# Kernel optimization log

Hardware: AMD Instinct MI355X
Metric: run time of the kernel (lower is better)

The kernel has to match this reference:

```python
import jax, jax.numpy as jnp
import numpy as np

DIM = 512
N_LAYERS = 2
N_HEADS = 8
HEAD_DIM = DIM // N_HEADS
VOCAB = 50257
MAX_SEQ = 2048
N_LEVELS = 3  # len(chunk_sizes)
HID = 4 * DIM
B, S = 2, 1024
STD = 0.02
EPS = 1e-5


def setup_inputs() -> dict:
    key = jax.random.key(0)
    ks = jax.random.split(key, 12)
    f32 = jnp.float32
    inp = {}
    inp["input_ids"] = jax.random.randint(ks[0], (B, S), 0, VOCAB)
    inp["tok_emb"] = jax.random.normal(ks[1], (VOCAB, DIM), f32) * STD  # tied with head
    inp["pos_emb"] = jax.random.normal(ks[2], (MAX_SEQ, DIM), f32) * STD
    # attention projections, stored [in, out] so y = x @ W (math-equivalent to torch x @ W.T)
    inp["Wq"] = jax.random.normal(ks[3], (N_LAYERS, DIM, DIM), f32) * STD
    inp["Wk"] = jax.random.normal(ks[4], (N_LAYERS, DIM, DIM), f32) * STD
    inp["Wv"] = jax.random.normal(ks[5], (N_LAYERS, DIM, DIM), f32) * STD
    inp["Wo"] = jax.random.normal(ks[6], (N_LAYERS, DIM, DIM), f32) * STD
    # layer norms
    inp["ln1_g"] = jnp.ones((N_LAYERS, DIM), f32)
    inp["ln1_b"] = jnp.zeros((N_LAYERS, DIM), f32)
    inp["ln2_g"] = jnp.ones((N_LAYERS, DIM), f32)
    inp["ln2_b"] = jnp.zeros((N_LAYERS, DIM), f32)
    inp["lnf_g"] = jnp.ones((DIM,), f32)
    inp["lnf_b"] = jnp.zeros((DIM,), f32)
    # continuum memory system: N_LEVELS chained MLPs per layer
    inp["W1"] = jax.random.normal(ks[7], (N_LAYERS, N_LEVELS, DIM, HID), f32) * STD
    inp["b1"] = jnp.zeros((N_LAYERS, N_LEVELS, HID), f32)
    inp["W2"] = jax.random.normal(ks[8], (N_LAYERS, N_LEVELS, HID, DIM), f32) * STD
    inp["b2"] = jnp.zeros((N_LAYERS, N_LEVELS, DIM), f32)
    return inp


def layer_norm(x, g, b):
    mu = jnp.mean(x, axis=-1, keepdims=True)
    var = jnp.var(x, axis=-1, keepdims=True)
    return (x - mu) / jnp.sqrt(var + EPS) * g + b


def linear_attention_with_memory(x, Wq, Wk, Wv, Wo):
    # x: [B, S, D]. Fast-weight recurrence: M_t = M_{t-1} + v_t k_t^T ; y_t = M_t q_t
    Bsz, Slen, D = x.shape
    H, hd = N_HEADS, HEAD_DIM

    def proj(W):  # -> [S, B, H, hd] (time-major for scan)
        return jnp.moveaxis((x @ W).reshape(Bsz, Slen, H, hd), 1, 0)

    q, k, v = proj(Wq), proj(Wk), proj(Wv)
    M0 = jnp.zeros((Bsz, H, hd, hd), x.dtype)

    def step(M, qkv):
        q_t, k_t, v_t = qkv
        M = M + jnp.einsum('bhd,bhk->bhdk', v_t, k_t)
        y_t = jnp.einsum('bhdk,bhk->bhd', M, q_t)
        return M, y_t

    _, ys = jax.lax.scan(step, M0, (q, k, v))  # ys: [S, B, H, hd]
    y = jnp.moveaxis(ys, 0, 1).reshape(Bsz, Slen, D)
    return y @ Wo


def cms(x, W1, b1, W2, b2):
    # chained MLP levels (dropout=0 / eval mode)
    for m in range(W1.shape[0]):
        x = jax.nn.gelu(x @ W1[m] + b1[m]) @ W2[m] + b2[m]
    return x


def reference(input_ids, tok_emb, pos_emb, Wq, Wk, Wv, Wo,
              ln1_g, ln1_b, ln2_g, ln2_b, lnf_g, lnf_b,
              W1, b1, W2, b2):
    Bsz, Slen = input_ids.shape
    x = tok_emb[input_ids] + pos_emb[:Slen][None, :, :]
    for l in range(Wq.shape[0]):
        x = x + linear_attention_with_memory(layer_norm(x, ln1_g[l], ln1_b[l]),
                                             Wq[l], Wk[l], Wv[l], Wo[l])
        x = x + cms(layer_norm(x, ln2_g[l], ln2_b[l]), W1[l], b1[l], W2[l], b2[l])
    x = layer_norm(x, lnf_g, lnf_b)
    logits = x @ tok_emb.T  # tied head
    return logits
```

## Files before the change

kernel.cpp:

```cpp
#include <hip/hip_runtime.h>
#include <hip/hip_bf16.h>
#include <cstdint>

using bf16 = __hip_bfloat16;
typedef __attribute__((ext_vector_type(8))) __bf16 bf16x8;
typedef __attribute__((ext_vector_type(4))) float f32x4;
typedef __attribute__((ext_vector_type(4))) unsigned int u32x4;

#define SEQ    1024
#define BATCH  2
#define ROWS   (BATCH*SEQ)
#define DMODEL 512
#define HIDDEN 2048
#define NHEADS 8
#define HD     64
#define VOCABN 50257
#define CHUNK  32
#define NCHUNK (SEQ/CHUNK)
#define QKVW   1536

__device__ __forceinline__ float gelu_tanh(float x) {
  float u = 0.7978845608028654f * (x + 0.044715f * x * x * x);
  return 0.5f * x * (1.0f + tanhf(u));
}

template<int EPI>
__global__ __launch_bounds__(256, 2)
void gemm_bt(const bf16* __restrict__ A, const bf16* __restrict__ Bt,
             void* __restrict__ Cout, const float* __restrict__ bias,
             int M, int N, int K, int ldc, int ntn)
{
  __shared__ __align__(16) bf16 As[128 * 32];
  __shared__ __align__(16) bf16 Bs[128 * 32];
  const int t = threadIdx.x;
  const int lane = t & 63;
  const int w = t >> 6;
  const int wr = w >> 1, wc = w & 1;
  const int tile = blockIdx.x;
  const int tm = tile / ntn, tn = tile % ntn;

  f32x4 acc[4][4];
#pragma unroll
  for (int m = 0; m < 4; ++m)
#pragma unroll
    for (int n = 0; n < 4; ++n) acc[m][n] = (f32x4){0.f, 0.f, 0.f, 0.f};

  const int rA = lane & 15;
  const int kq = (lane >> 4) * 8;
  const size_t a_row0 = (size_t)tm * 128;
  const int b_row0 = tn * 128;

  for (int k0 = 0; k0 < K; k0 += 32) {
#pragma unroll
    for (int i = 0; i < 2; ++i) {
      int chunk = i * 256 + t;
      int row = chunk >> 2;
      int kc = (chunk & 3) * 8;
      const bf16* ga = A + (a_row0 + row) * K + k0 + kc;
      int brow = b_row0 + row; brow = brow < N ? brow : N - 1;
      const bf16* gb = Bt + (size_t)brow * K + k0 + kc;
      __builtin_amdgcn_global_load_lds(
          (const __attribute__((address_space(1))) unsigned int*)ga,
          (__attribute__((address_space(3))) unsigned int*)(As + (size_t)(i * 256 + w * 64) * 8),
          16, 0, 0);
      __builtin_amdgcn_global_load_lds(
          (const __attribute__((address_space(1))) unsigned int*)gb,
          (__attribute__((address_space(3))) unsigned int*)(Bs + (size_t)(i * 256 + w * 64) * 8),
          16, 0, 0);
    }
    asm volatile("s_waitcnt vmcnt(0)" ::: "memory");
    __syncthreads();

    bf16x8 af[4], bfv[4];
#pragma unroll
    for (int m = 0; m < 4; ++m)
      af[m] = __builtin_bit_cast(bf16x8, *(const u32x4*)(As + (wr * 64 + m * 16 + rA) * 32 + kq));
#pragma unroll
    for (int n = 0; n < 4; ++n)
      bfv[n] = __builtin_bit_cast(bf16x8, *(const u32x4*)(Bs + (wc * 64 + n * 16 + rA) * 32 + kq));
#pragma unroll
    for (int m = 0; m < 4; ++m)
#pragma unroll
      for (int n = 0; n < 4; ++n)
        acc[m][n] = __builtin_amdgcn_mfma_f32_16x16x32_bf16(af[m], bfv[n], acc[m][n], 0, 0, 0);
    __syncthreads();
  }

#pragma unroll
  for (int m = 0; m < 4; ++m) {
    const int row = tm * 128 + wr * 64 + m * 16 + (lane >> 4) * 4;
#pragma unroll
    for (int n = 0; n < 4; ++n) {
      const int col = tn * 128 + wc * 64 + n * 16 + (lane & 15);
      if (col < N) {
#pragma unroll
        for (int r = 0; r < 4; ++r) {
          float v = acc[m][n][r];
          if (EPI == 2) { v += bias[col]; v = gelu_tanh(v); }
          size_t off = (size_t)(row + r) * ldc + col;
          if (EPI == 0) ((float*)Cout)[off] = v;
          else ((bf16*)Cout)[off] = __float2bfloat16(v);
        }
      }
    }
  }
}

__global__ __launch_bounds__(256, 2)
void gemm_bt_sk(const bf16* __restrict__ A, const bf16* __restrict__ Bt,
                float* __restrict__ part, int M, int N, int K, int Ks, int ntn)
{
  __shared__ __align__(16) bf16 As[128 * 32];
  __shared__ __align__(16) bf16 Bs[128 * 32];
  const int t = threadIdx.x;
  const int lane = t & 63;
  const int w = t >> 6;
  const int wr = w >> 1, wc = w & 1;
  const int tile = blockIdx.x;
  const int tm = tile / ntn, tn = tile % ntn;
  const int s = blockIdx.y;

  f32x4 acc[4][4];
#pragma unroll
  for (int m = 0; m < 4; ++m)
#pragma unroll
    for (int n = 0; n < 4; ++n) acc[m][n] = (f32x4){0.f, 0.f, 0.f, 0.f};

  const int rA = lane & 15;
  const int kq = (lane >> 4) * 8;
  const size_t a_row0 = (size_t)tm * 128;
  const int b_row0 = tn * 128;
  const int kbeg = s * Ks, kend = kbeg + Ks;

  for (int k0 = kbeg; k0 < kend; k0 += 32) {
#pragma unroll
    for (int i = 0; i < 2; ++i) {
      int chunk = i * 256 + t;
      int row = chunk >> 2;
      int kc = (chunk & 3) * 8;
      const bf16* ga = A + (a_row0 + row) * K + k0 + kc;
      const bf16* gb = Bt + (size_t)(b_row0 + row) * K + k0 + kc;
      __builtin_amdgcn_global_load_lds(
          (const __attribute__((address_space(1))) unsigned int*)ga,
          (__attribute__((address_space(3))) unsigned int*)(As + (size_t)(i * 256 + w * 64) * 8),
          16, 0, 0);
      __builtin_amdgcn_global_load_lds(
          (const __attribute__((address_space(1))) unsigned int*)gb,
          (__attribute__((address_space(3))) unsigned int*)(Bs + (size_t)(i * 256 + w * 64) * 8),
          16, 0, 0);
    }
    asm volatile("s_waitcnt vmcnt(0)" ::: "memory");
    __syncthreads();

    bf16x8 af[4], bfv[4];
#pragma unroll
    for (int m = 0; m < 4; ++m)
      af[m] = __builtin_bit_cast(bf16x8, *(const u32x4*)(As + (wr * 64 + m * 16 + rA) * 32 + kq));
#pragma unroll
    for (int n = 0; n < 4; ++n)
      bfv[n] = __builtin_bit_cast(bf16x8, *(const u32x4*)(Bs + (wc * 64 + n * 16 + rA) * 32 + kq));
#pragma unroll
    for (int m = 0; m < 4; ++m)
#pragma unroll
      for (int n = 0; n < 4; ++n)
        acc[m][n] = __builtin_amdgcn_mfma_f32_16x16x32_bf16(af[m], bfv[n], acc[m][n], 0, 0, 0);
    __syncthreads();
  }

  float* o = part + (size_t)s * M * N;
#pragma unroll
  for (int m = 0; m < 4; ++m) {
    const int row = tm * 128 + wr * 64 + m * 16 + (lane >> 4) * 4;
#pragma unroll
    for (int n = 0; n < 4; ++n) {
      const int col = tn * 128 + wc * 64 + n * 16 + (lane & 15);
#pragma unroll
      for (int r = 0; r < 4; ++r)
        o[(size_t)(row + r) * N + col] = acc[m][n][r];
    }
  }
}

__global__ __launch_bounds__(256)
void reduce_bias_bf16(const float* __restrict__ part, bf16* __restrict__ out,
                      const float* __restrict__ bias)
{
  int i = blockIdx.x * 256 + threadIdx.x;
  const float4* p4 = (const float4*)part;
  const size_t str = (size_t)ROWS * DMODEL / 4;
  float4 v = p4[i];
  float4 v1 = p4[i + str], v2 = p4[i + 2 * str], v3 = p4[i + 3 * str];
  v.x += v1.x + v2.x + v3.x; v.y += v1.y + v2.y + v3.y;
  v.z += v1.z + v2.z + v3.z; v.w += v1.w + v2.w + v3.w;
  float4 bb = ((const float4*)bias)[i & (DMODEL / 4 - 1)];
  v.x += bb.x; v.y += bb.y; v.z += bb.z; v.w += bb.w;
  union { bf16 h[4]; uint2 u; } cv;
  cv.h[0] = __float2bfloat16(v.x); cv.h[1] = __float2bfloat16(v.y);
  cv.h[2] = __float2bfloat16(v.z); cv.h[3] = __float2bfloat16(v.w);
  ((uint2*)out)[i] = cv.u;
}

template<bool BIAS>
__global__ __launch_bounds__(256)
void reduce_resid_ln(const float* __restrict__ part, float* __restrict__ x,
                     const float* __restrict__ bias, const float* __restrict__ g,
                     const float* __restrict__ b, bf16* __restrict__ xn)
{
  int lane = threadIdx.x & 63;
  int row = blockIdx.x * 4 + (threadIdx.x >> 6);
  const float4* p4 = (const float4*)part;
  const size_t str = (size_t)ROWS * DMODEL / 4;
  size_t base = (size_t)row * (DMODEL / 4) + lane * 2;
  float4 a0 = p4[base], a1 = p4[base + 1];
#pragma unroll
  for (int s = 1; s < 4; ++s) {
    float4 q0 = p4[base + s * str], q1 = p4[base + 1 + s * str];
    a0.x += q0.x; a0.y += q0.y; a0.z += q0.z; a0.w += q0.w;
    a1.x += q1.x; a1.y += q1.y; a1.z += q1.z; a1.w += q1.w;
  }
  if (BIAS) {
    float4 b0 = ((const float4*)bias)[lane * 2];
    float4 b1 = ((const float4*)bias)[lane * 2 + 1];
    a0.x += b0.x; a0.y += b0.y; a0.z += b0.z; a0.w += b0.w;
    a1.x += b1.x; a1.y += b1.y; a1.z += b1.z; a1.w += b1.w;
  }
  float4* xr = (float4*)(x + (size_t)row * DMODEL);
  float4 x0 = xr[lane * 2], x1 = xr[lane * 2 + 1];
  x0.x += a0.x; x0.y += a0.y; x0.z += a0.z; x0.w += a0.w;
  x1.x += a1.x; x1.y += a1.y; x1.z += a1.z; x1.w += a1.w;
  xr[lane * 2] = x0; xr[lane * 2 + 1] = x1;
  float s  = x0.x + x0.y + x0.z + x0.w + x1.x + x1.y + x1.z + x1.w;
  float ss = x0.x*x0.x + x0.y*x0.y + x0.z*x0.z + x0.w*x0.w
           + x1.x*x1.x + x1.y*x1.y + x1.z*x1.z + x1.w*x1.w;
#pragma unroll
  for (int off = 32; off > 0; off >>= 1) { s += __shfl_xor(s, off); ss += __shfl_xor(ss, off); }
  float mu = s * (1.f / DMODEL);
  float inv = rsqrtf(ss * (1.f / DMODEL) - mu * mu + 1e-5f);
  int c0 = lane * 8;
  float vv[8] = {x0.x, x0.y, x0.z, x0.w, x1.x, x1.y, x1.z, x1.w};
#pragma unroll
  for (int j = 0; j < 8; ++j)
    xn[(size_t)row * DMODEL + c0 + j] = __float2bfloat16((vv[j] - mu) * inv * g[c0 + j] + b[c0 + j]);
}

__global__ __launch_bounds__(256)
void embed_ln(const int* __restrict__ ids, const float* __restrict__ te,
              const float* __restrict__ pe, const float* __restrict__ g,
              const float* __restrict__ b, float* __restrict__ x, bf16* __restrict__ xn)
{
  int lane = threadIdx.x & 63;
  int row = blockIdx.x * 4 + (threadIdx.x >> 6);
  int sq = row & (SEQ - 1);
  int id = ids[row];
  const float4* tr = (const float4*)(te + (size_t)id * DMODEL);
  const float4* pr = (const float4*)(pe + (size_t)sq * DMODEL);
  float4 x0 = tr[lane * 2], x1 = tr[lane * 2 + 1];
  float4 p0 = pr[lane * 2], p1 = pr[lane * 2 + 1];
  x0.x += p0.x; x0.y += p0.y; x0.z += p0.z; x0.w += p0.w;
  x1.x += p1.x; x1.y += p1.y; x1.z += p1.z; x1.w += p1.w;
  float4* xr = (float4*)(x + (size_t)row * DMODEL);
  xr[lane * 2] = x0; xr[lane * 2 + 1] = x1;
  float s  = x0.x + x0.y + x0.z + x0.w + x1.x + x1.y + x1.z + x1.w;
  float ss = x0.x*x0.x + x0.y*x0.y + x0.z*x0.z + x0.w*x0.w
           + x1.x*x1.x + x1.y*x1.y + x1.z*x1.z + x1.w*x1.w;
#pragma unroll
  for (int off = 32; off > 0; off >>= 1) { s += __shfl_xor(s, off); ss += __shfl_xor(ss, off); }
  float mu = s * (1.f / DMODEL);
  float inv = rsqrtf(ss * (1.f / DMODEL) - mu * mu + 1e-5f);
  int c0 = lane * 8;
  float vv[8] = {x0.x, x0.y, x0.z, x0.w, x1.x, x1.y, x1.z, x1.w};
#pragma unroll
  for (int j = 0; j < 8; ++j)
    xn[(size_t)row * DMODEL + c0 + j] = __float2bfloat16((vv[j] - mu) * inv * g[c0 + j] + b[c0 + j]);
}

__global__ __launch_bounds__(256)
void transpose_cvt(const float* __restrict__ in, bf16* __restrict__ out, int R, int C)
{
  __shared__ float tile[32][33];
  int mat = blockIdx.z;
  const float* src = in + (size_t)mat * R * C;
  bf16* dst = out + (size_t)mat * R * C;
  int c0 = blockIdx.x * 32, r0 = blockIdx.y * 32;
  int tx = threadIdx.x, ty = threadIdx.y;
#pragma unroll
  for (int i = ty; i < 32; i += 8)
    tile[i][tx] = src[(size_t)(r0 + i) * C + c0 + tx];
  __syncthreads();
#pragma unroll
  for (int i = ty; i < 32; i += 8)
    dst[(size_t)(c0 + i) * R + r0 + tx] = __float2bfloat16(tile[tx][i]);
}

__global__ __launch_bounds__(256)
void transpose_qkv(const float* __restrict__ Wq, const float* __restrict__ Wk,
                   const float* __restrict__ Wv, bf16* __restrict__ out)
{
  __shared__ float tile[32][33];
  int z = blockIdx.z;
  int l = z / 3, p = z % 3;
  const float* src = (p == 0 ? Wq : (p == 1 ? Wk : Wv)) + (size_t)l * DMODEL * DMODEL;
  bf16* dst = out + (size_t)l * QKVW * DMODEL + (size_t)p * DMODEL * DMODEL;
  int c0 = blockIdx.x * 32, r0 = blockIdx.y * 32;
  int tx = threadIdx.x, ty = threadIdx.y;
#pragma unroll
  for (int i = ty; i < 32; i += 8)
    tile[i][tx] = src[(size_t)(r0 + i) * DMODEL + c0 + tx];
  __syncthreads();
#pragma unroll
  for (int i = ty; i < 32; i += 8)
    dst[(size_t)(c0 + i) * DMODEL + r0 + tx] = __float2bfloat16(tile[tx][i]);
}

__global__ void cvt_bf16_k(const float* __restrict__ in, bf16* __restrict__ out, int n4)
{
  int i = blockIdx.x * 256 + threadIdx.x;
  if (i >= n4) return;
  float4 v = ((const float4*)in)[i];
  union { bf16 h[4]; uint2 u; } cv;
  cv.h[0] = __float2bfloat16(v.x); cv.h[1] = __float2bfloat16(v.y);
  cv.h[2] = __float2bfloat16(v.z); cv.h[3] = __float2bfloat16(v.w);
  ((uint2*)out)[i] = cv.u;
}

__global__ __launch_bounds__(256)
void scan_ktv(const float* __restrict__ qkv, float* __restrict__ ktv)
{
  int blk = blockIdx.x;
  int c = blk & (NCHUNK - 1), bh = blk >> 5;
  int b = bh >> 3, h = bh & 7;
  __shared__ float ks[CHUNK][64], vs[CHUNK][64];
  int t = threadIdx.x;
  size_t base = ((size_t)(b * SEQ + c * CHUNK)) * QKVW + h * HD;
#pragma unroll
  for (int i = 0; i < CHUNK * 64 / 256; ++i) {
    int idx = i * 256 + t;
    int s = idx >> 6, e = idx & 63;
    ks[s][e] = qkv[base + 512 + (size_t)s * QKVW + e];
    vs[s][e] = qkv[base + 1024 + (size_t)s * QKVW + e];
  }
  __syncthreads();
  int e = t >> 2, d0 = (t & 3) * 16;
  float acc[16];
#pragma unroll
  for (int j = 0; j < 16; ++j) acc[j] = 0.f;
  for (int s = 0; s < CHUNK; ++s) {
    float kv = ks[s][e];
#pragma unroll
    for (int j = 0; j < 16; ++j) acc[j] += kv * vs[s][d0 + j];
  }
  float* o = ktv + (size_t)blk * 4096 + e * 64 + d0;
#pragma unroll
  for (int j = 0; j < 16; ++j) o[j] = acc[j];
}

__global__ __launch_bounds__(256)
void scan_attn(const float* __restrict__ qkv, const float* __restrict__ ktv,
               bf16* __restrict__ y)
{
  int blk = blockIdx.x;
  int c = blk & (NCHUNK - 1), bh = blk >> 5;
  int b = bh >> 3, h = bh & 7;
  __shared__ float qs[CHUNK][65], ks[CHUNK][65], vs[CHUNK][65];
  __shared__ float Ss[CHUNK][CHUNK + 1];
  __shared__ float Ms[64][65];
  int t = threadIdx.x;
  size_t base = ((size_t)(b * SEQ + c * CHUNK)) * QKVW + h * HD;
#pragma unroll
  for (int i = 0; i < CHUNK * 64 / 256; ++i) {
    int idx = i * 256 + t;
    int s = idx >> 6, e = idx & 63;
    qs[s][e] = qkv[base + (size_t)s * QKVW + e];
    ks[s][e] = qkv[base + 512 + (size_t)s * QKVW + e];
    vs[s][e] = qkv[base + 1024 + (size_t)s * QKVW + e];
  }
  {
    int e = t >> 2, d0 = (t & 3) * 16;
    float mp[16];
#pragma unroll
    for (int j = 0; j < 16; ++j) mp[j] = 0.f;
    for (int cp = 0; cp < c; ++cp) {
      const float* p = ktv + ((size_t)bh * NCHUNK + cp) * 4096 + e * 64 + d0;
#pragma unroll
      for (int j = 0; j < 16; ++j) mp[j] += p[j];
    }
#pragma unroll
    for (int j = 0; j < 16; ++j) Ms[e][d0 + j] = mp[j];
  }
  __syncthreads();
  {
    int si = t >> 3, j0 = (t & 7) * 4;
    float sa[4] = {0.f, 0.f, 0.f, 0.f};
    for (int e = 0; e < 64; ++e) {
      float qv = qs[si][e];
#pragma unroll
      for (int j = 0; j < 4; ++j) sa[j] += qv * ks[j0 + j][e];
    }
#pragma unroll
    for (int j = 0; j < 4; ++j) Ss[si][j0 + j] = (j0 + j <= si) ? sa[j] : 0.f;
  }
  __syncthreads();
  {
    int si = t >> 3, d0 = (t & 7) * 8;
    float ya[8];
#pragma unroll
    for (int j = 0; j < 8; ++j) ya[j] = 0.f;
    for (int sp = 0; sp < CHUNK; ++sp) {
      float sv = Ss[si][sp];
#pragma unroll
      for (int j = 0; j < 8; ++j) ya[j] += sv * vs[sp][d0 + j];
    }
    for (int e = 0; e < 64; ++e) {
      float qv = qs[si][e];
#pragma unroll
      for (int j = 0; j < 8; ++j) ya[j] += qv * Ms[e][d0 + j];
    }
    bf16* o = y + ((size_t)(b * SEQ + c * CHUNK + si)) * DMODEL + h * HD + d0;
#pragma unroll
    for (int j = 0; j < 8; ++j) o[j] = __float2bfloat16(ya[j]);
  }
}

extern "C" void kernel_launch(void* const* d_in, const int* in_sizes, int n_in,
                              void* d_out, int out_size, void* d_ws, size_t ws_size,
                              hipStream_t stream)
{
  const int*   ids  = (const int*)  d_in[0];
  const float* tok  = (const float*)d_in[1];
  const float* pos  = (const float*)d_in[2];
  const float* Wq   = (const float*)d_in[3];
  const float* Wk   = (const float*)d_in[4];
  const float* Wv   = (const float*)d_in[5];
  const float* Wo   = (const float*)d_in[6];
  const float* ln1g = (const float*)d_in[7];
  const float* ln1b = (const float*)d_in[8];
  const float* ln2g = (const float*)d_in[9];
  const float* ln2b = (const float*)d_in[10];
  const float* lnfg = (const float*)d_in[11];
  const float* lnfb = (const float*)d_in[12];
  const float* W1   = (const float*)d_in[13];
  const float* b1   = (const float*)d_in[14];
  const float* W2   = (const float*)d_in[15];
  const float* b2   = (const float*)d_in[16];
  float* out = (float*)d_out;

  char* ws = (char*)d_ws;
  size_t off = 0;
  auto alloc = [&](size_t bytes) { void* p = ws + off; off += (bytes + 255) & ~(size_t)255; return p; };
  bf16* QKVt = (bf16*)alloc((size_t)2 * QKVW * 512 * 2);
  bf16* Wot  = (bf16*)alloc((size_t)2 * 512 * 512 * 2);
  bf16* W1t  = (bf16*)alloc((size_t)6 * 512 * 2048 * 2);
  bf16* W2t  = (bf16*)alloc((size_t)6 * 2048 * 512 * 2);
  bf16* tokb = (bf16*)alloc((size_t)VOCABN * 512 * 2);
  float* x   = (float*)alloc((size_t)ROWS * 512 * 4);
  bf16*  xn  = (bf16*) alloc((size_t)ROWS * 512 * 2);
  bf16*  tbuf= (bf16*) alloc((size_t)ROWS * 512 * 2);
  bf16*  hbuf= (bf16*) alloc((size_t)ROWS * 2048 * 2);
  float* qkvf= (float*)alloc((size_t)ROWS * QKVW * 4);
  bf16*  yb  = (bf16*) alloc((size_t)ROWS * 512 * 2);
  float* ktv = (float*)alloc((size_t)16 * NCHUNK * 4096 * 4);
  float* part= (float*)alloc((size_t)4 * ROWS * 512 * 4);

  dim3 tb(32, 8);
  transpose_qkv<<<dim3(16, 16, 6), tb, 0, stream>>>(Wq, Wk, Wv, QKVt);
  transpose_cvt<<<dim3(16, 16, 2), tb, 0, stream>>>(Wo, Wot, 512, 512);
  transpose_cvt<<<dim3(64, 16, 6), tb, 0, stream>>>(W1, W1t, 512, 2048);
  transpose_cvt<<<dim3(16, 64, 6), tb, 0, stream>>>(W2, W2t, 2048, 512);
  int n4 = VOCABN * 512 / 4;
  cvt_bf16_k<<<(n4 + 255) / 256, 256, 0, stream>>>(tok, tokb, n4);

  embed_ln<<<ROWS / 4, 256, 0, stream>>>(ids, tok, pos, ln1g, ln1b, x, xn);

  for (int l = 0; l < 2; ++l) {
    gemm_bt<0><<<dim3((ROWS / 128) * (QKVW / 128)), 256, 0, stream>>>(
        xn, QKVt + (size_t)l * QKVW * 512, qkvf, nullptr, ROWS, QKVW, 512, QKVW, QKVW / 128);
    scan_ktv<<<16 * NCHUNK, 256, 0, stream>>>(qkvf, ktv);
    scan_attn<<<16 * NCHUNK, 256, 0, stream>>>(qkvf, ktv, yb);
    gemm_bt_sk<<<dim3((ROWS / 128) * 4, 4), 256, 0, stream>>>(
        yb, Wot + (size_t)l * 512 * 512, part, ROWS, 512, 512, 128, 4);
    reduce_resid_ln<false><<<ROWS / 4, 256, 0, stream>>>(
        part, x, nullptr, ln2g + l * 512, ln2b + l * 512, xn);

    const bf16* cur = xn;
    for (int m = 0; m < 3; ++m) {
      int lm = l * 3 + m;
      gemm_bt<2><<<dim3((ROWS / 128) * (2048 / 128)), 256, 0, stream>>>(
          cur, W1t + (size_t)lm * 2048 * 512, hbuf, b1 + (size_t)lm * 2048,
          ROWS, 2048, 512, 2048, 2048 / 128);
      gemm_bt_sk<<<dim3((ROWS / 128) * 4, 4), 256, 0, stream>>>(
          hbuf, W2t + (size_t)lm * 512 * 2048, part, ROWS, 512, 2048, 512, 4);
      if (m < 2) {
        reduce_bias_bf16<<<ROWS * 512 / 4 / 256, 256, 0, stream>>>(part, tbuf, b2 + (size_t)lm * 512);
        cur = tbuf;
      } else {
        const float* g = (l == 0) ? (ln1g + 512) : lnfg;
        const float* b = (l == 0) ? (ln1b + 512) : lnfb;
        reduce_resid_ln<true><<<ROWS / 4, 256, 0, stream>>>(part, x, b2 + (size_t)lm * 512, g, b, xn);
      }
    }
  }

  gemm_bt<0><<<dim3((ROWS / 128) * ((VOCABN + 127) / 128)), 256, 0, stream>>>(
      xn, tokb, out, nullptr, ROWS, VOCABN, 512, VOCABN, (VOCABN + 127) / 128);
}
```

Measured before the change: 667.5 us.

## Add 256x256-tile pipelined head GEMM with direct-to-LDS loads for vocab logits

Replaces the 128x128-tile generic GEMM for the tied vocab head with a dedicated 512-thread kernel. It uses 256x256 tiles, 128 KB of dynamic LDS holding double-buffered 64-wide K stages, and global_load_lds async copies interleaved with MFMA phases under explicit waitcnt and barriers. The larger tiles and pipelining aim to raise operand reuse and overlap loads with compute on the dominant logits GEMM. The costs are one block per CU because of the LDS size, more waste on the padded last vocab tile, and reliance on a fallback launch if the attribute or launch fails.

```diff
diff --git a/kernel.cpp b/kernel.cpp
--- a/kernel.cpp
+++ b/kernel.cpp
@@ -22,6 +22,136 @@
 __device__ __forceinline__ float gelu_tanh(float x) {
   float u = 0.7978845608028654f * (x + 0.044715f * x * x * x);
   return 0.5f * x * (1.0f + tanhf(u));
+}
+
+__global__ __launch_bounds__(512, 2)
+void head_gemm8(const bf16* __restrict__ A, const bf16* __restrict__ Bt,
+                float* __restrict__ C, int N, int ntn)
+{
+  constexpr int NT = 8;
+  extern __shared__ char smem[];
+  bf16* Al = (bf16*)smem;
+  bf16* Bl = (bf16*)(smem + 65536);
+  const int t = threadIdx.x, lane = t & 63;
+  const int w = t >> 6, wm = w >> 2, wn = w & 3;
+  const int tm = blockIdx.x / ntn, tn = blockIdx.x % ntn;
+  const int arow0 = tm * 256, brow0 = tn * 256;
+  const int klocal = (lane >> 4) * 16;
+
+  f32x4 acc[2][2][4][2];
+#pragma unroll
+  for (int i = 0; i < 2; ++i)
+#pragma unroll
+    for (int j = 0; j < 2; ++j)
+#pragma unroll
+      for (int m = 0; m < 4; ++m)
+#pragma unroll
+        for (int n = 0; n < 2; ++n) acc[i][j][m][n] = (f32x4){0.f, 0.f, 0.f, 0.f};
+
+  auto stageA = [&](int s, int half, bf16* dstbuf) {
+#pragma unroll
+    for (int rep = 0; rep < 2; ++rep) {
+      int slot = rep * 512 + t;
+      int row = slot >> 3, ko = slot & 7;
+      const bf16* src = A + (size_t)(arow0 + half * 128 + row) * 512 + s * 64 + ko * 8;
+      bf16* dst = dstbuf + (half * 128 + row) * 64 + ko * 8;
+      __builtin_amdgcn_global_load_lds(
+          (const __attribute__((address_space(1))) unsigned int*)src,
+          (__attribute__((address_space(3))) unsigned int*)dst, 16, 0, 0);
+    }
+  };
+  auto stageB = [&](int s, int half, bf16* dstbuf) {
+#pragma unroll
+    for (int rep = 0; rep < 2; ++rep) {
+      int slot = rep * 512 + t;
+      int row = slot >> 3, ko = slot & 7;
+      int br = brow0 + half * 128 + row; br = br < N ? br : N - 1;
+      const bf16* src = Bt + (size_t)br * 512 + s * 64 + ko * 8;
+      bf16* dst = dstbuf + (half * 128 + row) * 64 + ko * 8;
+      __builtin_amdgcn_global_load_lds(
+          (const __attribute__((address_space(1))) unsigned int*)src,
+          (__attribute__((address_space(3))) unsigned int*)dst, 16, 0, 0);
+    }
+  };
+
+  bf16* Ac = Al;
+  bf16* Bc = Bl;
+  bf16* An = Al + 16384;
+  bf16* Bn = Bl + 16384;
+
+  stageA(0, 0, Ac); stageB(0, 0, Bc); stageA(0, 1, Ac); stageB(0, 1, Bc);
+  stageA(1, 0, An); stageB(1, 0, Bn);
+  asm volatile("s_waitcnt vmcnt(4)" ::: "memory");
+  asm volatile("s_barrier" ::: "memory");
+
+#define PH(MH, NH, AC, BC, STAGE_STMT, WAIT_STMT) do {                          \
+    bf16x8 a_[4][2], b_[2][2];                                                  \
+    _Pragma("unroll") for (int fm = 0; fm < 4; ++fm) {                          \
+      const char* ap = (const char*)(AC) +                                      \
+          ((MH) * 128 + wm * 64 + fm * 16 + (lane & 15)) * 128 + klocal;        \
+      a_[fm][0] = __builtin_bit_cast(bf16x8, *(const u32x4*)ap);                \
+      a_[fm][1] = __builtin_bit_cast(bf16x8, *(const u32x4*)(ap + 64));         \
+    }                                                                           \
+    _Pragma("unroll") for (int fn = 0; fn < 2; ++fn) {                          \
+      const char* bp = (const char*)(BC) +                                      \
+          ((NH) * 128 + wn * 32 + fn * 16 + (lane & 15)) * 128 + klocal;        \
+      b_[fn][0] = __builtin_bit_cast(bf16x8, *(const u32x4*)bp);                \
+      b_[fn][1] = __builtin_bit_cast(bf16x8, *(const u32x4*)(bp + 64));         \
+    }                                                                           \
+    STAGE_STMT;                                                                 \
+    asm volatile("s_barrier" ::: "memory");                                     \
+    asm volatile("s_waitcnt lgkmcnt(0)" ::: "memory");                          \
+    __builtin_amdgcn_sched_barrier(0);                                          \
+    __builtin_amdgcn_s_setprio(1);                                              \
+    _Pragma("unroll") for (int fm = 0; fm < 4; ++fm)                            \
+      _Pragma("unroll") for (int fn = 0; fn < 2; ++fn) {                        \
+        acc[MH][NH][fm][fn] = __builtin_amdgcn_mfma_f32_16x16x32_bf16(          \
+            a_[fm][0], b_[fn][0], acc[MH][NH][fm][fn], 0, 0, 0);                \
+        acc[MH][NH][fm][fn] = __builtin_amdgcn_mfma_f32_16x16x32_bf16(          \
+            a_[fm][1], b_[fn][1], acc[MH][NH][fm][fn], 0, 0, 0);                \
+      }                                                                         \
+    __builtin_amdgcn_s_setprio(0);                                              \
+    WAIT_STMT;                                                                  \
+    asm volatile("s_barrier" ::: "memory");                                     \
+  } while (0)
+
+#pragma unroll
+  for (int I = 0; I < NT / 2; ++I) {
+    const int u = 2 * I;
+    PH(0, 0, Ac, Bc, { stageA(u + 1, 1, An); }, {});
+    PH(0, 1, Ac, Bc, { stageB(u + 1, 1, Bn); }, {});
+    PH(1, 0, Ac, Bc, { if (u + 2 < NT) stageA(u + 2, 0, Ac); }, {});
+    PH(1, 1, Ac, Bc, { if (u + 2 < NT) stageB(u + 2, 0, Bc); },
+       { if (u + 2 < NT) asm volatile("s_waitcnt vmcnt(4)" ::: "memory");
+         else            asm volatile("s_waitcnt vmcnt(0)" ::: "memory"); });
+    PH(0, 0, An, Bn, { if (u + 2 < NT) stageA(u + 2, 1, Ac); }, {});
+    PH(0, 1, An, Bn, { if (u + 2 < NT) stageB(u + 2, 1, Bc); }, {});
+    PH(1, 0, An, Bn, { if (u + 3 < NT) stageA(u + 3, 0, An); }, {});
+    PH(1, 1, An, Bn, { if (u + 3 < NT) stageB(u + 3, 0, Bn); },
+       { if (u + 2 < NT) {
+           if (u + 3 < NT) asm volatile("s_waitcnt vmcnt(4)" ::: "memory");
+           else            asm volatile("s_waitcnt vmcnt(0)" ::: "memory");
+         } });
+  }
+#undef PH
+
+#pragma unroll
+  for (int mh = 0; mh < 2; ++mh)
+#pragma unroll
+    for (int fm = 0; fm < 4; ++fm) {
+      int row = arow0 + mh * 128 + wm * 64 + fm * 16 + (lane >> 4) * 4;
+#pragma unroll
+      for (int nh = 0; nh < 2; ++nh)
+#pragma unroll
+        for (int fn = 0; fn < 2; ++fn) {
+          int col = brow0 + nh * 128 + wn * 32 + fn * 16 + (lane & 15);
+          if (col < N) {
+#pragma unroll
+            for (int r = 0; r < 4; ++r)
+              C[(size_t)(row + r) * N + col] = acc[mh][nh][fm][fn][r];
+          }
+        }
+    }
 }
 
 template<int EPI>
@@ -500,6 +630,12 @@
     }
   }
 
-  gemm_bt<0><<<dim3((ROWS / 128) * ((VOCABN + 127) / 128)), 256, 0, stream>>>(
-      xn, tokb, out, nullptr, ROWS, VOCABN, 512, VOCABN, (VOCABN + 127) / 128);
-}
+  int ntn_h = (VOCABN + 255) / 256;
+  (void)hipFuncSetAttribute((const void*)head_gemm8,
+                            hipFuncAttributeMaxDynamicSharedMemorySize, 131072);
+  head_gemm8<<<dim3((ROWS / 256) * ntn_h), 512, 131072, stream>>>(xn, tokb, out, VOCABN, ntn_h);
+  if (hipGetLastError() != hipSuccess) {
+    gemm_bt<0><<<dim3((ROWS / 128) * ((VOCABN + 127) / 128)), 256, 0, stream>>>(
+        xn, tokb, out, nullptr, ROWS, VOCABN, 512, VOCABN, (VOCABN + 127) / 128);
+  }
+}
```

Result: slower. 720.4 us (+7.9%).
